# Kernel optimization log

Hardware: AMD Instinct MI355X
Metric: run time of the kernel (lower is better)

## Reference

```python
import jax, jax.numpy as jnp
import numpy as np

B, D, H = 8192, 1024, 1024


def _linear_init(key, shape, fan_in):
    bound = 1.0 / np.sqrt(fan_in)
    return jax.random.uniform(key, shape, jnp.float32, -bound, bound)


def setup_inputs() -> dict:
    key = jax.random.key(0)
    ks = jax.random.split(key, 20)
    inp = {
        "x": jax.random.normal(ks[0], (B, D), jnp.float32),
        "h_prev": jax.random.normal(ks[1], (B, H), jnp.float32),
        "c_prev": jax.random.normal(ks[2], (B, H), jnp.float32),
        "C_prev": jax.random.normal(ks[3], (B, H), jnp.float32),
        "n_prev": jax.random.uniform(ks[4], (B, H), jnp.float32),
        "m_prev": jax.random.normal(ks[5], (B, H), jnp.float32),
    }
    # input projections Wz/Wi/Wf/Wo: Linear(D -> H) with bias
    for i, g in enumerate("ziofo"[:4]):
        pass
    names = ["z", "i", "f", "o"]
    for j, g in enumerate(names):
        inp[f"W{g}"] = _linear_init(ks[6 + j], (H, D), D)
        inp[f"b{g}"] = _linear_init(ks[10 + j], (H,), D)
        inp[f"R{g}"] = _linear_init(ks[14 + j], (H, H), H)  # no bias
    return inp


def reference(x, h_prev, c_prev, C_prev, n_prev, m_prev,
              Wz, bz, Wi, bi, Wf, bf, Wo, bo,
              Rz, Ri, Rf, Ro):
    # Batch the 4 input projections and 4 recurrent projections into 2 GEMMs.
    Wcat = jnp.concatenate([Wi, Wf, Wo, Wz], axis=0)        # [4H, D]
    bcat = jnp.concatenate([bi, bf, bo, bz], axis=0)        # [4H]
    Rcat = jnp.concatenate([Ri, Rf, Ro, Rz], axis=0)        # [4H, H]
    pre = x @ Wcat.T + bcat + h_prev @ Rcat.T               # [B, 4H]
    pi, pf, po, pz = jnp.split(pre, 4, axis=1)

    i = jnp.exp(pi)
    f = jax.nn.sigmoid(pf)
    o = jax.nn.sigmoid(po)
    z = jnp.tanh(pz)

    c = f * c_prev + i * z
    n = f * n_prev + i
    m = jnp.maximum(jnp.log(f) + m_prev, pi)  # log(exp(pi)) == pi
    h = o * (c / n)
    return (h, c, C_prev, n, m)
```

## Files before the change

kernel.cpp:

```cpp
#include <hip/hip_runtime.h>


#define B_SZ 8192
#define D_SZ 1024
#define H_SZ 1024
#define K_SZ 2048
#define N4H  4096

typedef __attribute__((ext_vector_type(4))) float f32x4;
typedef _Float16 f16;
typedef __attribute__((ext_vector_type(8))) f16 f16x8;
typedef unsigned short u16;
typedef __attribute__((ext_vector_type(4))) unsigned short u16x4;

static __device__ __forceinline__ u16 f2h(float f) {
    f16 h = (f16)f;
    return __builtin_bit_cast(unsigned short, h);
}

static __device__ __forceinline__ void load_lds16(const void* g, void* l) {
    __builtin_amdgcn_global_load_lds(
        (const __attribute__((address_space(1))) void*)g,
        (__attribute__((address_space(3))) void*)l, 16, 0, 0);
}

__global__ void convert_A(const float* __restrict__ x, const float* __restrict__ h,
                          u16* __restrict__ A) {
    const size_t nvec = (size_t)B_SZ * K_SZ / 4;
    const size_t stride = (size_t)gridDim.x * blockDim.x;
    for (size_t v = (size_t)blockIdx.x * blockDim.x + threadIdx.x; v < nvec; v += stride) {
        size_t e = v * 4;
        size_t row = e >> 11;
        int col = (int)(e & 2047);
        const float* src = (col < D_SZ) ? (x + row * D_SZ + col)
                                        : (h + row * H_SZ + (col - D_SZ));
        f32x4 val = *(const f32x4*)src;
        u16x4 o;
        o[0] = f2h(val[0]); o[1] = f2h(val[1]); o[2] = f2h(val[2]); o[3] = f2h(val[3]);
        *(u16x4*)(A + e) = o;
    }
}

__global__ void convert_W(const float* __restrict__ Wi, const float* __restrict__ Wf,
                          const float* __restrict__ Wo, const float* __restrict__ Wz,
                          const float* __restrict__ Ri, const float* __restrict__ Rf,
                          const float* __restrict__ Ro, const float* __restrict__ Rz,
                          u16* __restrict__ Wb) {
    const size_t nvec = (size_t)N4H * K_SZ / 4;
    const size_t stride = (size_t)gridDim.x * blockDim.x;
    for (size_t v = (size_t)blockIdx.x * blockDim.x + threadIdx.x; v < nvec; v += stride) {
        size_t e = v * 4;
        size_t r = e >> 11;
        int col = (int)(e & 2047);
        int g = (int)(r >> 4) & 3;
        int j = (int)((r >> 6) << 4) | (int)(r & 15);
        const float* Wg = (g == 0) ? Wi : (g == 1) ? Wf : (g == 2) ? Wo : Wz;
        const float* Rg = (g == 0) ? Ri : (g == 1) ? Rf : (g == 2) ? Ro : Rz;
        const float* src = (col < D_SZ) ? (Wg + (size_t)j * D_SZ + col)
                                        : (Rg + (size_t)j * H_SZ + (col - D_SZ));
        f32x4 val = *(const f32x4*)src;
        u16x4 o;
        o[0] = f2h(val[0]); o[1] = f2h(val[1]); o[2] = f2h(val[2]); o[3] = f2h(val[3]);
        *(u16x4*)(Wb + e) = o;
    }
}

__global__ __launch_bounds__(256, 2)
void gemm_fused(const u16* __restrict__ A, const u16* __restrict__ W,
                const float* __restrict__ c_prev, const float* __restrict__ n_prev,
                const float* __restrict__ m_prev,
                const float* __restrict__ bi, const float* __restrict__ bfv,
                const float* __restrict__ bo, const float* __restrict__ bz,
                float* __restrict__ out) {
    __shared__ u16 lA[128 * 64];
    __shared__ u16 lB[128 * 64];

    const int tid = threadIdx.x;
    const int w  = tid >> 6;
    const int l  = tid & 63;
    const int wm = w >> 1;
    const int wn = w & 1;
    const int m0 = blockIdx.x * 128;
    const int n0 = blockIdx.y * 128;

    const int lrow8 = l >> 3;
    const int lseg  = (l & 7) ^ lrow8;

    const int fr = l & 15;
    const int kq = l >> 4;

    f32x4 acc[4][4] = {};

    for (int kt = 0; kt < K_SZ; kt += 64) {
#pragma unroll
        for (int r = 0; r < 4; ++r) {
            int rowA = r * 32 + w * 8 + lrow8;
            const u16* gA = A + (size_t)(m0 + rowA) * K_SZ + kt + lseg * 8;
            load_lds16(gA, (char*)lA + (r * 32 + w * 8) * 128);
            const u16* gB = W + (size_t)(n0 + rowA) * K_SZ + kt + lseg * 8;
            load_lds16(gB, (char*)lB + (r * 32 + w * 8) * 128);
        }
        __syncthreads();

#pragma unroll
        for (int ks = 0; ks < 2; ++ks) {
            f16x8 af[4], bfr[4];
#pragma unroll
            for (int mi = 0; mi < 4; ++mi) {
                int row = wm * 64 + mi * 16 + fr;
                int seg = (ks * 4 + kq) ^ (row & 7);
                af[mi] = *(const f16x8*)&lA[row * 64 + seg * 8];
            }
#pragma unroll
            for (int ni = 0; ni < 4; ++ni) {
                int row = wn * 64 + ni * 16 + fr;
                int seg = (ks * 4 + kq) ^ (row & 7);
                bfr[ni] = *(const f16x8*)&lB[row * 64 + seg * 8];
            }
#pragma unroll
            for (int mi = 0; mi < 4; ++mi)
#pragma unroll
                for (int ni = 0; ni < 4; ++ni)
                    acc[mi][ni] = __builtin_amdgcn_mfma_f32_16x16x32_f16(
                        af[mi], bfr[ni], acc[mi][ni], 0, 0, 0);
        }
        __syncthreads();
    }

    const size_t BH = (size_t)B_SZ * H_SZ;
    const int j = ((n0 + wn * 64) >> 6) * 16 + fr;
    const float bvi = bi[j], bvf = bfv[j], bvo = bo[j], bvz = bz[j];

#pragma unroll
    for (int mi = 0; mi < 4; ++mi) {
        const int rbase = m0 + wm * 64 + mi * 16 + kq * 4;
#pragma unroll
        for (int r2 = 0; r2 < 4; ++r2) {
            const size_t idx = (size_t)(rbase + r2) * H_SZ + j;
            float pi = acc[mi][0][r2] + bvi;
            float pf = acc[mi][1][r2] + bvf;
            float po = acc[mi][2][r2] + bvo;
            float pz = acc[mi][3][r2] + bvz;
            float iv = __expf(pi);
            float fv = 1.0f / (1.0f + __expf(-pf));
            float ov = 1.0f / (1.0f + __expf(-po));
            float e2 = __expf(2.0f * pz);
            float zv = 1.0f - 2.0f / (e2 + 1.0f);
            float cv = fv * c_prev[idx] + iv * zv;
            float nv = fv * n_prev[idx] + iv;
            float mv = fmaxf(__logf(fv) + m_prev[idx], pi);
            out[idx]          = ov * (cv / nv);
            out[BH + idx]     = cv;
            out[3 * BH + idx] = nv;
            out[4 * BH + idx] = mv;
        }
    }
}

extern "C" void kernel_launch(void* const* d_in, const int* in_sizes, int n_in,
                              void* d_out, int out_size, void* d_ws, size_t ws_size,
                              hipStream_t stream) {
    const float* x      = (const float*)d_in[0];
    const float* h_prev = (const float*)d_in[1];
    const float* c_prev = (const float*)d_in[2];
    const float* C_prev = (const float*)d_in[3];
    const float* n_prev = (const float*)d_in[4];
    const float* m_prev = (const float*)d_in[5];
    const float* Wz = (const float*)d_in[6];
    const float* bz = (const float*)d_in[7];
    const float* Rz = (const float*)d_in[8];
    const float* Wi = (const float*)d_in[9];
    const float* bi = (const float*)d_in[10];
    const float* Ri = (const float*)d_in[11];
    const float* Wf = (const float*)d_in[12];
    const float* bf = (const float*)d_in[13];
    const float* Rf = (const float*)d_in[14];
    const float* Wo = (const float*)d_in[15];
    const float* bo = (const float*)d_in[16];
    const float* Ro = (const float*)d_in[17];
    float* out = (float*)d_out;

    const size_t BH = (size_t)B_SZ * H_SZ;

    u16* Abuf = (u16*)d_ws;
    u16* Wbuf = (u16*)((char*)d_ws + (size_t)32 * 1024 * 1024);

    convert_A<<<2048, 256, 0, stream>>>(x, h_prev, Abuf);
    convert_W<<<2048, 256, 0, stream>>>(Wi, Wf, Wo, Wz, Ri, Rf, Ro, Rz, Wbuf);

    hipMemcpyAsync(out + 2 * BH, C_prev, BH * sizeof(float),
                   hipMemcpyDeviceToDevice, stream);

    gemm_fused<<<dim3(B_SZ / 128, N4H / 128), 256, 0, stream>>>(
        Abuf, Wbuf, c_prev, n_prev, m_prev, bi, bf, bo, bz, out);
}
```

Measured before the change: 225.8 us.

## Triple-buffer LDS with async prefetch, 256x128 tiles, XCD-aware block mapping

Rewrites the GEMM main loop to keep three LDS stages and issue global-to-LDS loads for tile t+2 while tile t is computed. Waits use explicit vmcnt counters instead of a full sync before and after each tile. Block tiles grow to 256x128 with 512 threads (8 waves), and a 1D grid is remapped so each XCD handles a contiguous slice of N to improve L2 reuse. s_setprio is raised around the MFMA bursts. This adds LDS usage (about 144KB per block) and relies on the hand-tuned vmcnt counts being correct.

```diff
diff --git a/kernel.cpp b/kernel.cpp
--- a/kernel.cpp
+++ b/kernel.cpp
@@ -6,6 +6,7 @@
 #define H_SZ 1024
 #define K_SZ 2048
 #define N4H  4096
+#define NT   32
 
 typedef __attribute__((ext_vector_type(4))) float f32x4;
 typedef _Float16 f16;
@@ -65,75 +66,118 @@
     }
 }
 
-__global__ __launch_bounds__(256, 2)
+__global__ __launch_bounds__(512, 2)
 void gemm_fused(const u16* __restrict__ A, const u16* __restrict__ W,
                 const float* __restrict__ c_prev, const float* __restrict__ n_prev,
                 const float* __restrict__ m_prev,
                 const float* __restrict__ bi, const float* __restrict__ bfv,
                 const float* __restrict__ bo, const float* __restrict__ bz,
                 float* __restrict__ out) {
-    __shared__ u16 lA[128 * 64];
-    __shared__ u16 lB[128 * 64];
+    __shared__ u16 lA[3][256 * 64];
+    __shared__ u16 lB[3][128 * 64];
 
     const int tid = threadIdx.x;
-    const int w  = tid >> 6;
-    const int l  = tid & 63;
-    const int wm = w >> 1;
-    const int wn = w & 1;
-    const int m0 = blockIdx.x * 128;
-    const int n0 = blockIdx.y * 128;
+    const int w   = tid >> 6;
+    const int l   = tid & 63;
+    const int wmm = w >> 1;
+    const int wn  = w & 1;
+
+    const int xcd = blockIdx.x & 7;
+    const int loc = blockIdx.x >> 3;
+    const int bm  = loc & 31;
+    const int bn  = xcd * 4 + (loc >> 5);
+    const int m0  = bm * 256;
+    const int n0r = bn * 128;
 
     const int lrow8 = l >> 3;
-    const int lseg  = (l & 7) ^ lrow8;
+    const int lcol  = l & 7;
+    const int srow  = w * 8 + lrow8;
+    const int gsegoff = (lcol ^ lrow8) * 8;
+
+    const u16* pA[4];
+#pragma unroll
+    for (int q = 0; q < 4; ++q)
+        pA[q] = A + (size_t)(m0 + q * 64 + srow) * K_SZ + gsegoff;
+    const u16* pB[2];
+#pragma unroll
+    for (int q = 0; q < 2; ++q)
+        pB[q] = W + (size_t)(n0r + q * 64 + srow) * K_SZ + gsegoff;
 
     const int fr = l & 15;
     const int kq = l >> 4;
 
     f32x4 acc[4][4] = {};
 
-    for (int kt = 0; kt < K_SZ; kt += 64) {
-#pragma unroll
-        for (int r = 0; r < 4; ++r) {
-            int rowA = r * 32 + w * 8 + lrow8;
-            const u16* gA = A + (size_t)(m0 + rowA) * K_SZ + kt + lseg * 8;
-            load_lds16(gA, (char*)lA + (r * 32 + w * 8) * 128);
-            const u16* gB = W + (size_t)(n0 + rowA) * K_SZ + kt + lseg * 8;
-            load_lds16(gB, (char*)lB + (r * 32 + w * 8) * 128);
+    auto stage_a = [&](int q, int kt, int slot) {
+        load_lds16(pA[q] + kt * 64,
+                   (char*)&lA[slot][0] + (q * 64 + w * 8) * 128);
+    };
+    auto stage_b = [&](int q, int kt, int slot) {
+        load_lds16(pB[q] + kt * 64,
+                   (char*)&lB[slot][0] + (q * 64 + w * 8) * 128);
+    };
+
+    auto do_phase = [&](int slot, int ks) {
+        f16x8 af[4], bfr[4];
+#pragma unroll
+        for (int mi = 0; mi < 4; ++mi) {
+            int row = wmm * 64 + mi * 16 + fr;
+            int seg = (ks * 4 + kq) ^ (row & 7);
+            af[mi] = *(const f16x8*)&lA[slot][row * 64 + seg * 8];
         }
-        __syncthreads();
-
-#pragma unroll
-        for (int ks = 0; ks < 2; ++ks) {
-            f16x8 af[4], bfr[4];
-#pragma unroll
-            for (int mi = 0; mi < 4; ++mi) {
-                int row = wm * 64 + mi * 16 + fr;
-                int seg = (ks * 4 + kq) ^ (row & 7);
-                af[mi] = *(const f16x8*)&lA[row * 64 + seg * 8];
-            }
-#pragma unroll
-            for (int ni = 0; ni < 4; ++ni) {
-                int row = wn * 64 + ni * 16 + fr;
-                int seg = (ks * 4 + kq) ^ (row & 7);
-                bfr[ni] = *(const f16x8*)&lB[row * 64 + seg * 8];
-            }
-#pragma unroll
-            for (int mi = 0; mi < 4; ++mi)
-#pragma unroll
-                for (int ni = 0; ni < 4; ++ni)
-                    acc[mi][ni] = __builtin_amdgcn_mfma_f32_16x16x32_f16(
-                        af[mi], bfr[ni], acc[mi][ni], 0, 0, 0);
+#pragma unroll
+        for (int ni = 0; ni < 4; ++ni) {
+            int row = wn * 64 + ni * 16 + fr;
+            int seg = (ks * 4 + kq) ^ (row & 7);
+            bfr[ni] = *(const f16x8*)&lB[slot][row * 64 + seg * 8];
         }
-        __syncthreads();
-    }
+        __builtin_amdgcn_s_setprio(1);
+#pragma unroll
+        for (int mi = 0; mi < 4; ++mi)
+#pragma unroll
+            for (int ni = 0; ni < 4; ++ni)
+                acc[mi][ni] = __builtin_amdgcn_mfma_f32_16x16x32_f16(
+                    af[mi], bfr[ni], acc[mi][ni], 0, 0, 0);
+        __builtin_amdgcn_s_setprio(0);
+    };
+
+#pragma unroll
+    for (int q = 0; q < 4; ++q) stage_a(q, 0, 0);
+    stage_b(0, 0, 0); stage_b(1, 0, 0);
+#pragma unroll
+    for (int q = 0; q < 4; ++q) stage_a(q, 1, 1);
+    stage_b(0, 1, 1); stage_b(1, 1, 1);
+
+#define TILE_STEP(T, SC, SPF, PF, W6)                                        \
+    do {                                                                     \
+        if (W6) { asm volatile("s_waitcnt vmcnt(6)" ::: "memory"); }         \
+        else    { asm volatile("s_waitcnt vmcnt(0)" ::: "memory"); }         \
+        __builtin_amdgcn_s_barrier();                                        \
+        if (PF) { stage_a(0, (T) + 2, (SPF)); stage_a(1, (T) + 2, (SPF));    \
+                  stage_b(0, (T) + 2, (SPF)); }                              \
+        do_phase((SC), 0);                                                   \
+        if (PF) { stage_a(2, (T) + 2, (SPF)); stage_a(3, (T) + 2, (SPF));    \
+                  stage_b(1, (T) + 2, (SPF)); }                              \
+        do_phase((SC), 1);                                                   \
+    } while (0)
+
+#pragma unroll 1
+    for (int t = 0; t < 30; t += 3) {
+        TILE_STEP(t,     0, 2, true, true);
+        TILE_STEP(t + 1, 1, 0, true, true);
+        TILE_STEP(t + 2, 2, 1, true, true);
+    }
+    TILE_STEP(30, 0, 0, false, true);
+    TILE_STEP(31, 1, 0, false, false);
+#undef TILE_STEP
 
     const size_t BH = (size_t)B_SZ * H_SZ;
-    const int j = ((n0 + wn * 64) >> 6) * 16 + fr;
+    const int j = (bn * 2 + wn) * 16 + fr;
     const float bvi = bi[j], bvf = bfv[j], bvo = bo[j], bvz = bz[j];
 
 #pragma unroll
     for (int mi = 0; mi < 4; ++mi) {
-        const int rbase = m0 + wm * 64 + mi * 16 + kq * 4;
+        const int rbase = m0 + wmm * 64 + mi * 16 + kq * 4;
 #pragma unroll
         for (int r2 = 0; r2 < 4; ++r2) {
             const size_t idx = (size_t)(rbase + r2) * H_SZ + j;
@@ -191,6 +235,6 @@
     hipMemcpyAsync(out + 2 * BH, C_prev, BH * sizeof(float),
                    hipMemcpyDeviceToDevice, stream);
 
-    gemm_fused<<<dim3(B_SZ / 128, N4H / 128), 256, 0, stream>>>(
+    gemm_fused<<<dim3((B_SZ / 256) * (N4H / 128)), 512, 0, stream>>>(
         Abuf, Wbuf, c_prev, n_prev, m_prev, bi, bf, bo, bz, out);
 }
```

Result: slower. 273.8 us (+21.3%).

## Double-buffer LDS tiles to overlap global loads with MFMA compute

Applied to the files above, without the earlier changes.

Splits the shared-memory A/B tiles into two slots and prefetches the next K-tile into the other slot while the current one is consumed by MFMAs. Explicit vmcnt waits and raw barriers replace the two __syncthreads per iteration. It also raises wave priority around the MFMA block. This aims to hide global-to-LDS latency, at the cost of doubling LDS use (64KB per block), which may limit the two-blocks-per-CU occupancy target.

```diff
diff --git a/kernel.cpp b/kernel.cpp
--- a/kernel.cpp
+++ b/kernel.cpp
@@ -72,8 +72,8 @@
                 const float* __restrict__ bi, const float* __restrict__ bfv,
                 const float* __restrict__ bo, const float* __restrict__ bz,
                 float* __restrict__ out) {
-    __shared__ u16 lA[128 * 64];
-    __shared__ u16 lB[128 * 64];
+    __shared__ u16 lA[2][128 * 64];
+    __shared__ u16 lB[2][128 * 64];
 
     const int tid = threadIdx.x;
     const int w  = tid >> 6;
@@ -91,40 +91,60 @@
 
     f32x4 acc[4][4] = {};
 
-    for (int kt = 0; kt < K_SZ; kt += 64) {
+    auto stage = [&](int kt, int slot) {
 #pragma unroll
         for (int r = 0; r < 4; ++r) {
             int rowA = r * 32 + w * 8 + lrow8;
-            const u16* gA = A + (size_t)(m0 + rowA) * K_SZ + kt + lseg * 8;
-            load_lds16(gA, (char*)lA + (r * 32 + w * 8) * 128);
-            const u16* gB = W + (size_t)(n0 + rowA) * K_SZ + kt + lseg * 8;
-            load_lds16(gB, (char*)lB + (r * 32 + w * 8) * 128);
-        }
-        __syncthreads();
-
-#pragma unroll
-        for (int ks = 0; ks < 2; ++ks) {
-            f16x8 af[4], bfr[4];
-#pragma unroll
-            for (int mi = 0; mi < 4; ++mi) {
-                int row = wm * 64 + mi * 16 + fr;
-                int seg = (ks * 4 + kq) ^ (row & 7);
-                af[mi] = *(const f16x8*)&lA[row * 64 + seg * 8];
-            }
-#pragma unroll
-            for (int ni = 0; ni < 4; ++ni) {
-                int row = wn * 64 + ni * 16 + fr;
-                int seg = (ks * 4 + kq) ^ (row & 7);
-                bfr[ni] = *(const f16x8*)&lB[row * 64 + seg * 8];
-            }
-#pragma unroll
-            for (int mi = 0; mi < 4; ++mi)
-#pragma unroll
-                for (int ni = 0; ni < 4; ++ni)
-                    acc[mi][ni] = __builtin_amdgcn_mfma_f32_16x16x32_f16(
-                        af[mi], bfr[ni], acc[mi][ni], 0, 0, 0);
-        }
-        __syncthreads();
+            const u16* gA = A + (size_t)(m0 + rowA) * K_SZ + kt * 64 + lseg * 8;
+            load_lds16(gA, (char*)&lA[slot][0] + (r * 32 + w * 8) * 128);
+            const u16* gB = W + (size_t)(n0 + rowA) * K_SZ + kt * 64 + lseg * 8;
+            load_lds16(gB, (char*)&lB[slot][0] + (r * 32 + w * 8) * 128);
+        }
+    };
+
+    auto do_phase = [&](int slot, int ks) {
+        f16x8 af[4], bfr[4];
+#pragma unroll
+        for (int mi = 0; mi < 4; ++mi) {
+            int row = wm * 64 + mi * 16 + fr;
+            int seg = (ks * 4 + kq) ^ (row & 7);
+            af[mi] = *(const f16x8*)&lA[slot][row * 64 + seg * 8];
+        }
+#pragma unroll
+        for (int ni = 0; ni < 4; ++ni) {
+            int row = wn * 64 + ni * 16 + fr;
+            int seg = (ks * 4 + kq) ^ (row & 7);
+            bfr[ni] = *(const f16x8*)&lB[slot][row * 64 + seg * 8];
+        }
+        __builtin_amdgcn_s_setprio(1);
+#pragma unroll
+        for (int mi = 0; mi < 4; ++mi)
+#pragma unroll
+            for (int ni = 0; ni < 4; ++ni)
+                acc[mi][ni] = __builtin_amdgcn_mfma_f32_16x16x32_f16(
+                    af[mi], bfr[ni], acc[mi][ni], 0, 0, 0);
+        __builtin_amdgcn_s_setprio(0);
+    };
+
+    stage(0, 0);
+#pragma unroll 1
+    for (int t = 0; t < 32; t += 2) {
+        stage(t + 1, 1);
+        asm volatile("s_waitcnt vmcnt(8)" ::: "memory");
+        __builtin_amdgcn_s_barrier();
+        do_phase(0, 0);
+        do_phase(0, 1);
+        __builtin_amdgcn_s_barrier();
+        if (t + 2 < 32) {
+            stage(t + 2, 0);
+            asm volatile("s_waitcnt vmcnt(8)" ::: "memory");
+        } else {
+            asm volatile("s_waitcnt vmcnt(0)" ::: "memory");
+        }
+        __builtin_amdgcn_s_barrier();
+        do_phase(1, 0);
+        do_phase(1, 1);
+        __builtin_amdgcn_s_barrier();
     }
 
     const size_t BH = (size_t)B_SZ * H_SZ;
```

Result: slower. 242.6 us (+7.4%).

## Enlarge GEMM tile to 256x256 with double-buffered LDS and phased prefetch pipeline

Applied to the files above, without the earlier changes.

The fused GEMM now uses a 256x256 output tile with 512 threads (8 waves in a 2x4 layout) instead of 128x128 with 256 threads. LDS is double-buffered, and the K loop is split into four phases per tile. Each phase issues async global-to-LDS loads for upcoming A/B subtiles, interleaved with MFMA work, and uses explicit vmcnt waits, s_barrier and s_setprio. The goal is to hide global load latency and raise arithmetic intensity per block. The cost is 128KB of LDS per block, 32 accumulator tiles per wave, and a complex hand-tuned schedule whose occupancy and correctness depend on exact wait counts.

```diff
diff --git a/kernel.cpp b/kernel.cpp
--- a/kernel.cpp
+++ b/kernel.cpp
@@ -65,75 +65,129 @@
     }
 }
 
-__global__ __launch_bounds__(256, 2)
+__global__ __launch_bounds__(512, 2)
 void gemm_fused(const u16* __restrict__ A, const u16* __restrict__ W,
                 const float* __restrict__ c_prev, const float* __restrict__ n_prev,
                 const float* __restrict__ m_prev,
                 const float* __restrict__ bi, const float* __restrict__ bfv,
                 const float* __restrict__ bo, const float* __restrict__ bz,
                 float* __restrict__ out) {
-    __shared__ u16 lA[128 * 64];
-    __shared__ u16 lB[128 * 64];
+    __shared__ u16 lA[2][256 * 64];
+    __shared__ u16 lB[2][256 * 64];
 
     const int tid = threadIdx.x;
-    const int w  = tid >> 6;
-    const int l  = tid & 63;
-    const int wm = w >> 1;
-    const int wn = w & 1;
-    const int m0 = blockIdx.x * 128;
-    const int n0 = blockIdx.y * 128;
+    const int w   = tid >> 6;
+    const int l   = tid & 63;
+    const int wm  = w >> 2;
+    const int wn  = w & 3;
+    const int m0  = blockIdx.x * 256;
+    const int n0r = blockIdx.y * 256;
 
     const int lrow8 = l >> 3;
     const int lseg  = (l & 7) ^ lrow8;
+    const int laneOff = lrow8 * K_SZ + lseg * 8;
 
     const int fr = l & 15;
     const int kq = l >> 4;
 
-    f32x4 acc[4][4] = {};
-
-    for (int kt = 0; kt < K_SZ; kt += 64) {
-#pragma unroll
-        for (int r = 0; r < 4; ++r) {
-            int rowA = r * 32 + w * 8 + lrow8;
-            const u16* gA = A + (size_t)(m0 + rowA) * K_SZ + kt + lseg * 8;
-            load_lds16(gA, (char*)lA + (r * 32 + w * 8) * 128);
-            const u16* gB = W + (size_t)(n0 + rowA) * K_SZ + kt + lseg * 8;
-            load_lds16(gB, (char*)lB + (r * 32 + w * 8) * 128);
-        }
-        __syncthreads();
-
-#pragma unroll
-        for (int ks = 0; ks < 2; ++ks) {
-            f16x8 af[4], bfr[4];
-#pragma unroll
-            for (int mi = 0; mi < 4; ++mi) {
-                int row = wm * 64 + mi * 16 + fr;
-                int seg = (ks * 4 + kq) ^ (row & 7);
-                af[mi] = *(const f16x8*)&lA[row * 64 + seg * 8];
+    const u16* Abase = A + (size_t)m0 * K_SZ + laneOff;
+    const u16* Bbase = W + (size_t)n0r * K_SZ + laneOff;
+
+    auto stA = [&](int h, int kt, int d) {
+#pragma unroll
+        for (int r = 0; r < 2; ++r)
+            load_lds16(Abase + (size_t)(h * 128 + r * 64 + w * 8) * K_SZ + kt * 64,
+                       (char*)&lA[d][0] + (h * 128 + r * 64 + w * 8) * 128);
+    };
+    auto stB = [&](int h, int kt, int d) {
+#pragma unroll
+        for (int r = 0; r < 2; ++r)
+            load_lds16(Bbase + (size_t)(h * 128 + r * 64 + w * 8) * K_SZ + kt * 64,
+                       (char*)&lB[d][0] + (h * 128 + r * 64 + w * 8) * 128);
+    };
+
+    f32x4 acc[8][4] = {};
+    f16x8 bf[4][2];
+
+    auto rdB = [&](int d) {
+#pragma unroll
+        for (int ni = 0; ni < 4; ++ni)
+#pragma unroll
+            for (int ks = 0; ks < 2; ++ks) {
+                int row = wn * 64 + ni * 16 + fr;
+                int seg = (ks * 4 + kq) ^ (fr & 7);
+                bf[ni][ks] = *(const f16x8*)&lB[d][row * 64 + seg * 8];
             }
-#pragma unroll
-            for (int ni = 0; ni < 4; ++ni) {
-                int row = wn * 64 + ni * 16 + fr;
-                int seg = (ks * 4 + kq) ^ (row & 7);
-                bfr[ni] = *(const f16x8*)&lB[row * 64 + seg * 8];
-            }
-#pragma unroll
-            for (int mi = 0; mi < 4; ++mi)
-#pragma unroll
-                for (int ni = 0; ni < 4; ++ni)
-                    acc[mi][ni] = __builtin_amdgcn_mfma_f32_16x16x32_f16(
-                        af[mi], bfr[ni], acc[mi][ni], 0, 0, 0);
-        }
-        __syncthreads();
-    }
+    };
+
+#define PHASE(d, p, STAGE, TAILWAIT)                                          \
+    do {                                                                      \
+        f16x8 af[2][2];                                                       \
+        _Pragma("unroll")                                                     \
+        for (int mi2 = 0; mi2 < 2; ++mi2)                                     \
+            _Pragma("unroll")                                                 \
+            for (int ks = 0; ks < 2; ++ks) {                                  \
+                int row = wm * 128 + ((p) * 2 + mi2) * 16 + fr;               \
+                int seg = (ks * 4 + kq) ^ (fr & 7);                           \
+                af[mi2][ks] = *(const f16x8*)&lA[d][row * 64 + seg * 8];      \
+            }                                                                 \
+        if ((p) == 0) rdB(d);                                                 \
+        STAGE;                                                                \
+        __builtin_amdgcn_s_barrier();                                         \
+        __builtin_amdgcn_s_setprio(1);                                        \
+        _Pragma("unroll")                                                     \
+        for (int mi2 = 0; mi2 < 2; ++mi2)                                     \
+            _Pragma("unroll")                                                 \
+            for (int ni = 0; ni < 4; ++ni)                                    \
+                _Pragma("unroll")                                             \
+                for (int ks = 0; ks < 2; ++ks)                                \
+                    acc[(p) * 2 + mi2][ni] =                                  \
+                        __builtin_amdgcn_mfma_f32_16x16x32_f16(               \
+                            af[mi2][ks], bf[ni][ks], acc[(p) * 2 + mi2][ni],  \
+                            0, 0, 0);                                         \
+        __builtin_amdgcn_s_setprio(0);                                        \
+        TAILWAIT;                                                             \
+        __builtin_amdgcn_s_barrier();                                         \
+    } while (0)
+
+#define TILE_STEADY(t, d)                                                     \
+    do {                                                                      \
+        PHASE(d, 0, stA(0, (t) + 1, (d) ^ 1), (void)0);                       \
+        PHASE(d, 1, stA(1, (t) + 1, (d) ^ 1), (void)0);                       \
+        PHASE(d, 2, stB(0, (t) + 2, (d)), (void)0);                           \
+        PHASE(d, 3, stB(1, (t) + 2, (d)),                                     \
+              asm volatile("s_waitcnt vmcnt(4)" ::: "memory"));               \
+    } while (0)
+
+    stA(0, 0, 0); stA(1, 0, 0); stB(0, 0, 0); stB(1, 0, 0);
+    stB(0, 1, 1); stB(1, 1, 1);
+    asm volatile("s_waitcnt vmcnt(4)" ::: "memory");
+    __builtin_amdgcn_s_barrier();
+
+#pragma unroll 1
+    for (int i = 0; i < 15; ++i) {
+        int t = 2 * i;
+        TILE_STEADY(t, 0);
+        TILE_STEADY(t + 1, 1);
+    }
+    PHASE(0, 0, stA(0, 31, 1), (void)0);
+    PHASE(0, 1, stA(1, 31, 1), (void)0);
+    PHASE(0, 2, (void)0, (void)0);
+    PHASE(0, 3, (void)0, asm volatile("s_waitcnt vmcnt(0)" ::: "memory"));
+    PHASE(1, 0, (void)0, (void)0);
+    PHASE(1, 1, (void)0, (void)0);
+    PHASE(1, 2, (void)0, (void)0);
+    PHASE(1, 3, (void)0, (void)0);
+#undef TILE_STEADY
+#undef PHASE
 
     const size_t BH = (size_t)B_SZ * H_SZ;
-    const int j = ((n0 + wn * 64) >> 6) * 16 + fr;
+    const int j = ((n0r + wn * 64) >> 6) * 16 + fr;
     const float bvi = bi[j], bvf = bfv[j], bvo = bo[j], bvz = bz[j];
 
 #pragma unroll
-    for (int mi = 0; mi < 4; ++mi) {
-        const int rbase = m0 + wm * 64 + mi * 16 + kq * 4;
+    for (int mi = 0; mi < 8; ++mi) {
+        const int rbase = m0 + wm * 128 + mi * 16 + kq * 4;
 #pragma unroll
         for (int r2 = 0; r2 < 4; ++r2) {
             const size_t idx = (size_t)(rbase + r2) * H_SZ + j;
@@ -191,6 +245,6 @@
     hipMemcpyAsync(out + 2 * BH, C_prev, BH * sizeof(float),
                    hipMemcpyDeviceToDevice, stream);
 
-    gemm_fused<<<dim3(B_SZ / 128, N4H / 128), 256, 0, stream>>>(
+    gemm_fused<<<dim3(B_SZ / 256, N4H / 256), 512, 0, stream>>>(
         Abuf, Wbuf, c_prev, n_prev, m_prev, bi, bf, bo, bz, out);
 }
```

After: 245.8 us. 1.09x slower.
